# Optimization experiments

Measured on AMD Instinct MI355X. Metric: run time of the kernel, lower is better.

## Reference

```python
import jax, jax.numpy as jnp
import numpy as np

NUM_SAMPLES = 32  # S: Gibbs chains per datapoint


def setup_inputs() -> dict:
    key = jax.random.key(0)
    ks = jax.random.split(key, 6)
    N, F, M, C = 2048, 1024, 128, 100
    x = jax.random.normal(ks[0], (N, F), dtype=jnp.float32)
    y = jax.random.randint(ks[1], (N,), 0, C)
    alpha_0 = jax.random.normal(ks[2], (M,), dtype=jnp.float32)
    alpha = jax.random.normal(ks[3], (M, F), dtype=jnp.float32) * jnp.float32(2.0 / np.sqrt(F))
    beta_0 = jax.random.normal(ks[4], (C,), dtype=jnp.float32)
    beta = jax.random.normal(ks[5], (C, M), dtype=jnp.float32) * jnp.float32(2.0 / np.sqrt(M))
    return {"x": x, "y": y, "alpha_0": alpha_0, "alpha": alpha, "beta_0": beta_0, "beta": beta}


def _gibbs_and_loglik(x, y, alpha_0, alpha, beta_0, beta):
    S = NUM_SAMPLES
    N = x.shape[0]
    C, M = beta.shape
    y_onehot = jax.nn.one_hot(y, C, dtype=x.dtype)           # (N, C)

    # compute_linear_pi / compute_pi_pos (pi_pos is no_grad in original)
    linear_pi = alpha_0[None, :] + x @ alpha.T               # (N, M)
    pi_pos = jax.lax.stop_gradient(jax.nn.sigmoid(linear_pi))

    key = jax.random.key(42)
    k_init, k_gibbs = jax.random.split(key)

    # init_sample2: Z ~ 2*Bernoulli(pi_pos) - 1, sampled S times  (no_grad)
    Z0 = 2.0 * jax.random.bernoulli(k_init, pi_pos, (S, N, M)).astype(x.dtype) - 1.0

    beta_sg = jax.lax.stop_gradient(beta)
    beta0_sg = jax.lax.stop_gradient(beta_0)

    # class logits for current Z; maintained incrementally across Gibbs steps
    lin0 = beta0_sg[None, None, :] + jnp.einsum('snm,cm->snc', Z0, beta_sg)  # (S, N, C)

    order = jnp.asarray(np.random.RandomState(0).permutation(M))  # fixed Gibbs sweep order
    keys = jax.random.split(k_gibbs, M)

    def step(carry, inp):
        Z, lin = carry
        j, k = inp
        zj = jnp.take(Z, j, axis=2)           # (S, N) current value of coord j
        bj = jnp.take(beta_sg, j, axis=1)     # (C,)
        pij = jnp.take(pi_pos, j, axis=1)     # (N,)
        # logits if coord j were +1 / -1 (rank-1 update of lin)
        lin_pos = lin + (1.0 - zj)[..., None] * bj
        lin_neg = lin + (-1.0 - zj)[..., None] * bj
        g_pos = jnp.exp(jnp.einsum('nc,snc->sn', y_onehot, lin_pos)) / jnp.sum(jnp.exp(lin_pos), axis=2)
        g_neg = jnp.exp(jnp.einsum('nc,snc->sn', y_onehot, lin_neg)) / jnp.sum(jnp.exp(lin_neg), axis=2)
        num = g_pos * pij[None, :]
        p = num / (num + g_neg * (1.0 - pij)[None, :])
        znew = 2.0 * jax.random.bernoulli(k, p).astype(lin.dtype) - 1.0  # (S, N)
        lin = lin + (znew - zj)[..., None] * bj
        Z = jax.lax.dynamic_update_index_in_dim(Z, znew, j, axis=2)
        return (Z, lin), None

    (Z, _), _ = jax.lax.scan(step, (Z0, lin0), (order, keys))
    Z = jax.lax.stop_gradient(Z)

    # moments
    EI = jnp.mean((Z + 1.0) * 0.5, axis=0)                   # (N, M)
    EII = jnp.mean(Z, axis=0)                                # (N, M)
    linear_gamma = beta_0[None, None, :] + jnp.einsum('snm,cm->snc', Z, beta)
    EIII = jnp.mean(jax.nn.logsumexp(linear_gamma, axis=2), axis=0)  # (N,)

    TermI = jnp.sum(y_onehot * (beta_0[None, :] + EII @ beta.T))
    TermII = jnp.sum(EIII)
    TermIII = jnp.sum(EI * linear_pi)
    TermIV = jnp.sum(jax.nn.softplus(linear_pi))             # log(1 + exp(linear_pi)), stable
    return TermI - TermII + TermIII - TermIV


def reference(x, y, alpha_0, alpha, beta_0, beta):
    return _gibbs_and_loglik(x, y, alpha_0, alpha, beta_0, beta)
```

## Files before the change

### kernel.cpp

```cpp
#include <hip/hip_runtime.h>
#include <hip/hip_fp16.h>
#include <stdint.h>

#define Nn 2048
#define Ff 1024
#define Mm 128
#define Cc 100
#define Ss 32
#define NM (Nn * Mm)
#define ELS 132
#define SCP 128
#define TOFF 16400
#define ESC 0.015625f
#define ESCLOG 4.15888308336f

typedef short bf8 __attribute__((ext_vector_type(8)));
typedef float f32x4 __attribute__((ext_vector_type(4)));

__device__ __forceinline__ uint32_t hash32(uint32_t chain, uint32_t ctr) {
  uint32_t h = chain * 0x9E3779B9u ^ (ctr * 0x85EBCA6Bu);
  h ^= h >> 16; h *= 0x7FEB352Du;
  h ^= h >> 15; h *= 0x846CA68Bu;
  h ^= h >> 16;
  return h;
}
__device__ __forceinline__ float urand(uint32_t chain, uint32_t ctr) {
  return (float)(hash32(chain, ctr) >> 8) * (1.0f / 16777216.0f);
}
__device__ __forceinline__ uint32_t f2bf(float f) {
  uint32_t b = __builtin_bit_cast(uint32_t, f);
  return (b + 0x7FFFu + ((b >> 16) & 1u)) >> 16;
}
__device__ __forceinline__ float bf2f(uint16_t u) {
  uint32_t b = ((uint32_t)u) << 16;
  return __builtin_bit_cast(float, b);
}
__device__ __forceinline__ int cperm(int c) {
  return ((c >> 2) & 3) * 32 + (c >> 4) * 4 + (c & 3);
}

__global__ __launch_bounds__(256) void k_lingemm(const float* __restrict__ x,
                                                 const float* __restrict__ alpha,
                                                 uint16_t* __restrict__ lpib) {
  __shared__ uint4 sA[256];
  __shared__ uint4 sB[1024];
  const int t = threadIdx.x;
  const int mt = blockIdx.x >> 2;
  const int ks = blockIdx.x & 3;
  const int m0 = mt * 32;
  const int w = t >> 6;
  const int l = t & 63;

  f32x4 acc[2][2] = {{{0.f, 0.f, 0.f, 0.f}, {0.f, 0.f, 0.f, 0.f}},
                     {{0.f, 0.f, 0.f, 0.f}, {0.f, 0.f, 0.f, 0.f}}};

  for (int kk = 0; kk < 4; ++kk) {
    const int k0 = ks * 256 + kk * 64;
    __syncthreads();
    {
      int row = t >> 3, c = t & 7;
      const float* px = &x[(m0 + row) * Ff + k0 + c * 8];
      float4 f0 = *(const float4*)px;
      float4 f1 = *(const float4*)(px + 4);
      uint4 v;
      v.x = f2bf(f0.x) | (f2bf(f0.y) << 16);
      v.y = f2bf(f0.z) | (f2bf(f0.w) << 16);
      v.z = f2bf(f1.x) | (f2bf(f1.y) << 16);
      v.w = f2bf(f1.z) | (f2bf(f1.w) << 16);
      sA[row * 8 + (c ^ (row & 7))] = v;
      #pragma unroll
      for (int rr = 0; rr < 4; ++rr) {
        int idx = t + rr * 256;
        int rowb = idx >> 3, cb = idx & 7;
        const float* pa = &alpha[rowb * Ff + k0 + cb * 8];
        float4 g0 = *(const float4*)pa;
        float4 g1 = *(const float4*)(pa + 4);
        uint4 vb;
        vb.x = f2bf(g0.x) | (f2bf(g0.y) << 16);
        vb.y = f2bf(g0.z) | (f2bf(g0.w) << 16);
        vb.z = f2bf(g1.x) | (f2bf(g1.y) << 16);
        vb.w = f2bf(g1.z) | (f2bf(g1.w) << 16);
        sB[rowb * 8 + (cb ^ (rowb & 7))] = vb;
      }
    }
    __syncthreads();
    #pragma unroll
    for (int kc = 0; kc < 2; ++kc) {
      int chunk = kc * 4 + (l >> 4);
      bf8 av[2], bv[2];
      #pragma unroll
      for (int fm = 0; fm < 2; ++fm) {
        int row = fm * 16 + (l & 15);
        av[fm] = __builtin_bit_cast(bf8, sA[row * 8 + (chunk ^ (row & 7))]);
      }
      #pragma unroll
      for (int fn = 0; fn < 2; ++fn) {
        int rowb = w * 32 + fn * 16 + (l & 15);
        bv[fn] = __builtin_bit_cast(bf8, sB[rowb * 8 + (chunk ^ (rowb & 7))]);
      }
      #pragma unroll
      for (int fm = 0; fm < 2; ++fm)
        #pragma unroll
        for (int fn = 0; fn < 2; ++fn)
          acc[fm][fn] = __builtin_amdgcn_mfma_f32_16x16x32_bf16(av[fm], bv[fn], acc[fm][fn], 0, 0, 0);
    }
  }
  #pragma unroll
  for (int fm = 0; fm < 2; ++fm)
    #pragma unroll
    for (int fn = 0; fn < 2; ++fn)
      #pragma unroll
      for (int r = 0; r < 4; ++r) {
        int row = m0 + fm * 16 + (l >> 4) * 4 + r;
        int col = w * 32 + fn * 16 + (l & 15);
        lpib[ks * NM + row * Mm + col] = (uint16_t)f2bf(acc[fm][fn][r]);
      }
}

__global__ __launch_bounds__(512, 4) void k_gibbs(const float* __restrict__ beta0g,
                                                  const float* __restrict__ betag,
                                                  const int* __restrict__ yg,
                                                  const float* __restrict__ alpha0,
                                                  const uint16_t* __restrict__ lpib,
                                                  float* __restrict__ out) {
  __shared__ __attribute__((aligned(16))) char SM[74384];
  uint16_t* bsb = (uint16_t*)SM;
  float* b0p = (float*)(SM + 28672);
  __half* tab = (__half*)SM;
  float* elpi = (float*)(SM + 65600);
  float* lpil = (float*)(SM + 67712);
  uint32_t* zsl = (uint32_t*)(SM + 69760);
  float* lsel = (float*)(SM + 71808);
  float* red = (float*)(SM + 72320);
  int* yl = (int*)(SM + 74368);
  const int t = threadIdx.x;
  const int n0 = blockIdx.x * 4;
  const int lane = t & 63;

  for (int idx = t; idx < 112 * 32; idx += 512) {
    int row = idx >> 5, c4 = (idx & 31) * 4;
    float4 v = *(const float4*)&betag[row * Mm + c4];
    uint2 o;
    o.x = f2bf(v.x) | (f2bf(v.y) << 16);
    o.y = f2bf(v.z) | (f2bf(v.w) << 16);
    *(uint2*)&bsb[row * 128 + c4] = o;
  }
  if (t < 128) {
    b0p[cperm(t)] = (t < Cc) ? beta0g[t] : 0.0f;
  }
  {
    int nls = t >> 7, j = t & 127;
    int g = (n0 + nls) * Mm + j;
    float lv = bf2f(lpib[g]) + bf2f(lpib[NM + g]) + bf2f(lpib[2 * NM + g]) +
               bf2f(lpib[3 * NM + g]) + alpha0[j];
    lpil[nls * Mm + j] = lv;
    elpi[nls * ELS + j] = __expf(lv);
  }
  if (t < 4) yl[t] = yg[n0 + t];
  __syncthreads();

  const int li = lane & 15;
  const int h = lane >> 4;
  const int cl = (t >> 6) * 16 + li;
  const int nl = cl >> 5;
  const int s = cl & 31;
  const uint32_t chain = (uint32_t)((n0 + nl) * Ss + s);
  const int c0 = h * 32;
  const int yv = yl[nl];
  const int pyv = cperm(yv);

  uint32_t zw0, zw1, zw2, zw3;
  {
    uint32_t zz = 0;
    #pragma unroll 1
    for (int b5 = 0; b5 < 32; ++b5) {
      int mloc = (b5 + h * 8) & 31;
      int m = h * 32 + mloc;
      float u = urand(chain, (uint32_t)m);
      float el = elpi[nl * ELS + m];
      zz |= (u * (1.0f + el) < el) ? (1u << mloc) : 0u;
    }
    zw0 = (uint32_t)__shfl((int)zz, li + 0);
    zw1 = (uint32_t)__shfl((int)zz, li + 16);
    zw2 = (uint32_t)__shfl((int)zz, li + 32);
    zw3 = (uint32_t)__shfl((int)zz, li + 48);
  }

  f32x4 acc[7];
  #pragma unroll
  for (int T = 0; T < 7; ++T) acc[T] = (f32x4){0.f, 0.f, 0.f, 0.f};
  #pragma unroll
  for (int ks = 0; ks < 4; ++ks) {
    uint32_t zw = (ks == 0) ? zw0 : ((ks == 1) ? zw1 : ((ks == 2) ? zw2 : zw3));
    uint32_t bits8 = (zw >> (h * 8)) & 0xFFu;
    uint4 pk;
    {
      uint32_t p0 = ((bits8 >> 0) & 1u) ? 0x3F80u : 0xBF80u;
      uint32_t p1 = ((bits8 >> 1) & 1u) ? 0x3F80u : 0xBF80u;
      uint32_t p2 = ((bits8 >> 2) & 1u) ? 0x3F80u : 0xBF80u;
      uint32_t p3 = ((bits8 >> 3) & 1u) ? 0x3F80u : 0xBF80u;
      uint32_t p4 = ((bits8 >> 4) & 1u) ? 0x3F80u : 0xBF80u;
      uint32_t p5 = ((bits8 >> 5) & 1u) ? 0x3F80u : 0xBF80u;
      uint32_t p6 = ((bits8 >> 6) & 1u) ? 0x3F80u : 0xBF80u;
      uint32_t p7 = ((bits8 >> 7) & 1u) ? 0x3F80u : 0xBF80u;
      pk.x = p0 | (p1 << 16); pk.y = p2 | (p3 << 16);
      pk.z = p4 | (p5 << 16); pk.w = p6 | (p7 << 16);
    }
    bf8 B = __builtin_bit_cast(bf8, pk);
    #pragma unroll
    for (int T = 0; T < 7; ++T) {
      bf8 A = __builtin_bit_cast(bf8, *(const uint4*)&bsb[(T * 16 + li) * 128 + ks * 32 + h * 8]);
      acc[T] = __builtin_amdgcn_mfma_f32_16x16x32_bf16(A, B, acc[T], 0, 0, 0);
    }
  }

  const __half2 HZERO = __builtin_bit_cast(__half2, 0u);
  __half2 E2[16];
  #pragma unroll
  for (int k = 0; k < 14; ++k) {
    float2 b0v = *(const float2*)&b0p[c0 + 2 * k];
    float ea = __expf(acc[(2 * k) >> 2][(2 * k) & 3] + b0v.x) * ESC;
    float eb = __expf(acc[(2 * k + 1) >> 2][(2 * k + 1) & 3] + b0v.y) * ESC;
    E2[k] = __floats2half2_rn(ea, eb);
  }
  E2[14] = HZERO; E2[15] = HZERO;
  if (h != 0) { E2[12] = HZERO; E2[13] = HZERO; }

  float Sb;
  {
    const __half2 one2 = __floats2half2_rn(1.0f, 1.0f);
    __half2 a0 = HZERO, a1 = HZERO, a2 = HZERO, a3 = HZERO;
    #pragma unroll
    for (int k = 0; k < 4; ++k) {
      a0 = __hfma2(E2[4 * k + 0], one2, a0);
      a1 = __hfma2(E2[4 * k + 1], one2, a1);
      a2 = __hfma2(E2[4 * k + 2], one2, a2);
      a3 = __hfma2(E2[4 * k + 3], one2, a3);
    }
    __half2 sv = __hadd2(__hadd2(a0, a1), __hadd2(a2, a3));
    float d = __low2float(sv) + __high2float(sv);
    float d1 = d + __shfl_xor(d, 16);
    Sb = d1 + __shfl_xor(d1, 32);
  }

  __syncthreads();
  for (int idx = t; idx < 32 * Cc; idx += 512) {
    int j4 = idx / Cc;
    int c = idx - j4 * Cc;
    int p = cperm(c);
    float4 bv = *(const float4*)&betag[c * Mm + j4 * 4];
    int j = j4 * 4;
    tab[(j + 0) * SCP + p] = __float2half(__expf(2.0f * bv.x));
    tab[TOFF + (j + 0) * SCP + p] = __float2half(__expf(-2.0f * bv.x));
    tab[(j + 1) * SCP + p] = __float2half(__expf(2.0f * bv.y));
    tab[TOFF + (j + 1) * SCP + p] = __float2half(__expf(-2.0f * bv.y));
    tab[(j + 2) * SCP + p] = __float2half(__expf(2.0f * bv.z));
    tab[TOFF + (j + 2) * SCP + p] = __float2half(__expf(-2.0f * bv.z));
    tab[(j + 3) * SCP + p] = __float2half(__expf(2.0f * bv.w));
    tab[TOFF + (j + 3) * SCP + p] = __float2half(__expf(-2.0f * bv.w));
  }
  for (int idx = t; idx < Mm * 28; idx += 512) {
    int j = idx / 28;
    int c = Cc + (idx - j * 28);
    int p = cperm(c);
    tab[j * SCP + p] = __float2half(1.0f);
    tab[TOFF + j * SCP + p] = __float2half(1.0f);
  }
  __syncthreads();

  uint4 va[4], vb[4];
  auto pf = [&](uint4 (&dst)[4], uint32_t bit, int j) {
    const uint4* p4 = (const uint4*)(tab + (bit ? TOFF : 0) + j * SCP + c0);
    dst[0] = p4[0]; dst[1] = p4[1]; dst[2] = p4[2]; dst[3] = p4[3];
  };
  auto step = [&](uint4 (&v)[4], uint32_t zjp, float eyel, float u) -> uint32_t {
    __half2 a0 = HZERO, a1 = HZERO, a2 = HZERO, a3 = HZERO;
    #pragma unroll
    for (int k = 0; k < 4; ++k) {
      a0 = __hfma2(E2[4 * k + 0], __builtin_bit_cast(__half2, v[k].x), a0);
      a1 = __hfma2(E2[4 * k + 1], __builtin_bit_cast(__half2, v[k].y), a1);
      a2 = __hfma2(E2[4 * k + 2], __builtin_bit_cast(__half2, v[k].z), a2);
      a3 = __hfma2(E2[4 * k + 3], __builtin_bit_cast(__half2, v[k].w), a3);
    }
    __half2 sv = __hadd2(__hadd2(a0, a1), __hadd2(a2, a3));
    float d = __low2float(sv) + __high2float(sv);
    float d1 = d + __shfl_xor(d, 16);
    float D = d1 + __shfl_xor(d1, 32);
    float Spos = zjp ? Sb : D;
    float Sneg = zjp ? D : Sb;
    float odds = eyel * Sneg * __builtin_amdgcn_rcpf(Spos);
    uint32_t znp = (u * (1.0f + odds) < odds) ? 1u : 0u;
    if ((znp ^ zjp) != 0u) {
      #pragma unroll
      for (int k = 0; k < 4; ++k) {
        E2[4 * k + 0] = __hmul2(E2[4 * k + 0], __builtin_bit_cast(__half2, v[k].x));
        E2[4 * k + 1] = __hmul2(E2[4 * k + 1], __builtin_bit_cast(__half2, v[k].y));
        E2[4 * k + 2] = __hmul2(E2[4 * k + 2], __builtin_bit_cast(__half2, v[k].z));
        E2[4 * k + 3] = __hmul2(E2[4 * k + 3], __builtin_bit_cast(__half2, v[k].w));
      }
      Sb = D;
    }
    return znp;
  };

  pf(va, zw0 & 1u, 0);

  #pragma unroll 1
  for (int jb = 0; jb < Mm; jb += 4) {
    int w = jb >> 5;
    uint32_t zwv = (w == 0) ? zw0 : ((w == 1) ? zw1 : ((w == 2) ? zw2 : zw3));
    const int sh = jb & 31;
    uint32_t b0 = (zwv >> (sh + 0)) & 1u;
    uint32_t b1 = (zwv >> (sh + 1)) & 1u;
    uint32_t b2 = (zwv >> (sh + 2)) & 1u;
    uint32_t b3 = (zwv >> (sh + 3)) & 1u;
    uint32_t b4;
    if (sh == 28) {
      uint32_t nw = (w == 0) ? zw1 : ((w == 1) ? zw2 : ((w == 2) ? zw3 : 0u));
      b4 = nw & 1u;
    } else {
      b4 = (zwv >> (sh + 4)) & 1u;
    }
    float4 elv = *(const float4*)&elpi[nl * ELS + jb];
    float eyel0 = __half2float(tab[(jb + 0) * SCP + pyv]) * elv.x;
    float eyel1 = __half2float(tab[(jb + 1) * SCP + pyv]) * elv.y;
    float eyel2 = __half2float(tab[(jb + 2) * SCP + pyv]) * elv.z;
    float eyel3 = __half2float(tab[(jb + 3) * SCP + pyv]) * elv.w;
    uint32_t h1 = hash32(chain, 256u + (uint32_t)jb);
    uint32_t h2 = hash32(chain, 258u + (uint32_t)jb);
    float u0 = (float)(h1 & 0xFFFFu) * (1.0f / 65536.0f);
    float u1 = (float)(h1 >> 16) * (1.0f / 65536.0f);
    float u2 = (float)(h2 & 0xFFFFu) * (1.0f / 65536.0f);
    float u3 = (float)(h2 >> 16) * (1.0f / 65536.0f);

    pf(vb, b1, jb + 1);
    b0 = step(va, b0, eyel0, u0);
    pf(va, b2, jb + 2);
    b1 = step(vb, b1, eyel1, u1);
    pf(vb, b3, jb + 3);
    b2 = step(va, b2, eyel2, u2);
    pf(va, b4, (jb + 4) & 127);
    b3 = step(vb, b3, eyel3, u3);

    uint32_t nib = b0 | (b1 << 1) | (b2 << 2) | (b3 << 3);
    zwv = (zwv & ~(0xFu << sh)) | (nib << sh);
    if (w == 0) zw0 = zwv; else if (w == 1) zw1 = zwv;
    else if (w == 2) zw2 = zwv; else zw3 = zwv;
  }

  float Sf;
  {
    const __half2 one2 = __floats2half2_rn(1.0f, 1.0f);
    __half2 a0 = HZERO, a1 = HZERO, a2 = HZERO, a3 = HZERO;
    #pragma unroll
    for (int k = 0; k < 4; ++k) {
      a0 = __hfma2(E2[4 * k + 0], one2, a0);
      a1 = __hfma2(E2[4 * k + 1], one2, a1);
      a2 = __hfma2(E2[4 * k + 2], one2, a2);
      a3 = __hfma2(E2[4 * k + 3], one2, a3);
    }
    __half2 sv = __hadd2(__hadd2(a0, a1), __hadd2(a2, a3));
    float d = __low2float(sv) + __high2float(sv);
    float d1 = d + __shfl_xor(d, 16);
    Sf = d1 + __shfl_xor(d1, 32);
  }
  if (h == 0) {
    lsel[cl] = __logf(Sf) + ESCLOG;
    zsl[cl * 4 + 0] = zw0; zsl[cl * 4 + 1] = zw1;
    zsl[cl * 4 + 2] = zw2; zsl[cl * 4 + 3] = zw3;
  }
  __syncthreads();

  {
    int nl2 = t >> 7;
    int mp = t & 127;
    int wsel = mp >> 5, sh0 = mp & 31;
    int cnt = 0;
    #pragma unroll 1
    for (int s2 = 0; s2 < 32; ++s2)
      cnt += (int)((zsl[(nl2 * 32 + s2) * 4 + wsel] >> sh0) & 1u);
    float EI = (float)cnt * (1.0f / 32.0f);
    float EII = 2.0f * EI - 1.0f;
    float l = lpil[nl2 * Mm + mp];
    int yv2 = yl[nl2];
    float bb = betag[yv2 * Mm + mp];
    float sp = (l > 20.0f) ? l : __logf(1.0f + __expf(l));
    float term = EII * bb + EI * l - sp;
    if (t < 128) term -= lsel[t] * (1.0f / 32.0f);
    if (t < 4) term += beta0g[yl[t]];
    red[t] = term;
  }
  __syncthreads();
  for (int off = 256; off > 0; off >>= 1) {
    if (t < off) red[t] += red[t + off];
    __syncthreads();
  }
  if (t == 0) atomicAdd(out, red[0]);
}

extern "C" void kernel_launch(void* const* d_in, const int* in_sizes, int n_in,
                              void* d_out, int out_size, void* d_ws, size_t ws_size,
                              hipStream_t stream) {
  const float* x = (const float*)d_in[0];
  const int* y = (const int*)d_in[1];
  const float* alpha0 = (const float*)d_in[2];
  const float* alpha = (const float*)d_in[3];
  const float* beta0 = (const float*)d_in[4];
  const float* beta = (const float*)d_in[5];
  float* out = (float*)d_out;

  uint16_t* lpib = (uint16_t*)d_ws;

  hipMemsetAsync(d_out, 0, sizeof(float), stream);
  k_lingemm<<<256, 256, 0, stream>>>(x, alpha, lpib);
  k_gibbs<<<512, 512, 0, stream>>>(beta0, beta, y, alpha0, lpib, out);
}
```

Baseline: 104.0 us.

## Remap Gibbs chains to 4 adjacent lanes with DPP reductions and fdot2

Each Gibbs chain now lives on 4 adjacent lanes instead of 4 lanes strided by 16. That lets the per-step class-sum reduction use two DPP quad ops instead of two cross-lane shuffles. Half2 FMA accumulation is replaced with fdot2 into float accumulators, and the exp(±2β) table layout is swizzled per quarter-window to avoid LDS bank conflicts. Blocks grow to 1024 threads covering 8 datapoints, which needs more LDS per block and may reduce occupancy. The E2 values are redistributed with extra shuffles after the MFMA init.

Result: no change. 103.1 us (-0.8%).

```diff
diff --git a/kernel.cpp b/kernel.cpp
--- a/kernel.cpp
+++ b/kernel.cpp
@@ -10,12 +10,28 @@
 #define NM (Nn * Mm)
 #define ELS 132
 #define SCP 128
-#define TOFF 16400
+#define TOFF 16416
 #define ESC 0.015625f
 #define ESCLOG 4.15888308336f
 
+typedef _Float16 h2f __attribute__((ext_vector_type(2)));
 typedef short bf8 __attribute__((ext_vector_type(8)));
 typedef float f32x4 __attribute__((ext_vector_type(4)));
+
+__device__ __forceinline__ float qsum4(float x) {
+  int a = __builtin_amdgcn_update_dpp(0, __builtin_bit_cast(int, x), 0xB1, 0xF, 0xF, false);
+  float xf = x + __builtin_bit_cast(float, a);
+  int b = __builtin_amdgcn_update_dpp(0, __builtin_bit_cast(int, xf), 0x4E, 0xF, 0xF, false);
+  return xf + __builtin_bit_cast(float, b);
+}
+
+__device__ __forceinline__ float dot2f(h2f a, h2f b, float c) {
+#if __has_builtin(__builtin_amdgcn_fdot2)
+  return __builtin_amdgcn_fdot2(a, b, c, false);
+#else
+  return fmaf((float)a[0], (float)b[0], fmaf((float)a[1], (float)b[1], c));
+#endif
+}
 
 __device__ __forceinline__ uint32_t hash32(uint32_t chain, uint32_t ctr) {
   uint32_t h = chain * 0x9E3779B9u ^ (ctr * 0x85EBCA6Bu);
@@ -37,6 +53,10 @@
 }
 __device__ __forceinline__ int cperm(int c) {
   return ((c >> 2) & 3) * 32 + (c >> 4) * 4 + (c & 3);
+}
+__device__ __forceinline__ int swz(int p) {
+  int win = p >> 5, o = p & 31;
+  return win * 32 + (((o >> 3) + win) & 3) * 8 + (o & 7);
 }
 
 __global__ __launch_bounds__(256) void k_lingemm(const float* __restrict__ x,
@@ -117,37 +137,37 @@
       }
 }
 
-__global__ __launch_bounds__(512, 4) void k_gibbs(const float* __restrict__ beta0g,
-                                                  const float* __restrict__ betag,
-                                                  const int* __restrict__ yg,
-                                                  const float* __restrict__ alpha0,
-                                                  const uint16_t* __restrict__ lpib,
-                                                  float* __restrict__ out) {
-  __shared__ __attribute__((aligned(16))) char SM[74384];
+__global__ __launch_bounds__(1024, 4) void k_gibbs(const float* __restrict__ beta0g,
+                                                   const float* __restrict__ betag,
+                                                   const int* __restrict__ yg,
+                                                   const float* __restrict__ alpha0,
+                                                   const uint16_t* __restrict__ lpib,
+                                                   float* __restrict__ out) {
+  __shared__ __attribute__((aligned(16))) char SM[79584];
   uint16_t* bsb = (uint16_t*)SM;
-  float* b0p = (float*)(SM + 28672);
   __half* tab = (__half*)SM;
   float* elpi = (float*)(SM + 65600);
-  float* lpil = (float*)(SM + 67712);
-  uint32_t* zsl = (uint32_t*)(SM + 69760);
-  float* lsel = (float*)(SM + 71808);
-  float* red = (float*)(SM + 72320);
-  int* yl = (int*)(SM + 74368);
+  float* lpil = (float*)(SM + 69824);
+  uint32_t* zsl = (uint32_t*)(SM + 73920);
+  float* lsel = (float*)(SM + 78016);
+  int* yl = (int*)(SM + 79040);
+  float* b0p = (float*)(SM + 79072);
+  float* red = (float*)(SM + 65600);
+
   const int t = threadIdx.x;
-  const int n0 = blockIdx.x * 4;
-  const int lane = t & 63;
-
-  for (int idx = t; idx < 112 * 32; idx += 512) {
+  const int n0 = blockIdx.x * 8;
+  const int L = t & 63;
+
+  for (int idx = t; idx < 112 * 32; idx += 1024) {
     int row = idx >> 5, c4 = (idx & 31) * 4;
-    float4 v = *(const float4*)&betag[row * Mm + c4];
+    int rr = (row < Cc) ? row : 0;
+    float4 v = *(const float4*)&betag[rr * Mm + c4];
     uint2 o;
     o.x = f2bf(v.x) | (f2bf(v.y) << 16);
     o.y = f2bf(v.z) | (f2bf(v.w) << 16);
     *(uint2*)&bsb[row * 128 + c4] = o;
   }
-  if (t < 128) {
-    b0p[cperm(t)] = (t < Cc) ? beta0g[t] : 0.0f;
-  }
+  if (t < 128) b0p[cperm(t)] = (t < Cc) ? beta0g[t] : 0.0f;
   {
     int nls = t >> 7, j = t & 127;
     int g = (n0 + nls) * Mm + j;
@@ -156,34 +176,26 @@
     lpil[nls * Mm + j] = lv;
     elpi[nls * ELS + j] = __expf(lv);
   }
-  if (t < 4) yl[t] = yg[n0 + t];
+  if (t < 8) yl[t] = yg[n0 + t];
   __syncthreads();
 
-  const int li = lane & 15;
-  const int h = lane >> 4;
-  const int cl = (t >> 6) * 16 + li;
+  const int cl = t >> 2;
+  const int hq = t & 3;
   const int nl = cl >> 5;
   const int s = cl & 31;
   const uint32_t chain = (uint32_t)((n0 + nl) * Ss + s);
-  const int c0 = h * 32;
   const int yv = yl[nl];
-  const int pyv = cperm(yv);
-
-  uint32_t zw0, zw1, zw2, zw3;
-  {
-    uint32_t zz = 0;
+
+  uint32_t zz = 0;
+  {
     #pragma unroll 1
     for (int b5 = 0; b5 < 32; ++b5) {
-      int mloc = (b5 + h * 8) & 31;
-      int m = h * 32 + mloc;
+      int mloc = (b5 + hq * 8) & 31;
+      int m = hq * 32 + mloc;
       float u = urand(chain, (uint32_t)m);
       float el = elpi[nl * ELS + m];
       zz |= (u * (1.0f + el) < el) ? (1u << mloc) : 0u;
     }
-    zw0 = (uint32_t)__shfl((int)zz, li + 0);
-    zw1 = (uint32_t)__shfl((int)zz, li + 16);
-    zw2 = (uint32_t)__shfl((int)zz, li + 32);
-    zw3 = (uint32_t)__shfl((int)zz, li + 48);
   }
 
   f32x4 acc[7];
@@ -191,8 +203,8 @@
   for (int T = 0; T < 7; ++T) acc[T] = (f32x4){0.f, 0.f, 0.f, 0.f};
   #pragma unroll
   for (int ks = 0; ks < 4; ++ks) {
-    uint32_t zw = (ks == 0) ? zw0 : ((ks == 1) ? zw1 : ((ks == 2) ? zw2 : zw3));
-    uint32_t bits8 = (zw >> (h * 8)) & 0xFFu;
+    uint32_t zw = (uint32_t)__shfl((int)zz, ((L & 15) << 2) | ks, 64);
+    uint32_t bits8 = (zw >> ((L >> 4) * 8)) & 0xFFu;
     uint4 pk;
     {
       uint32_t p0 = ((bits8 >> 0) & 1u) ? 0x3F80u : 0xBF80u;
@@ -209,83 +221,98 @@
     bf8 B = __builtin_bit_cast(bf8, pk);
     #pragma unroll
     for (int T = 0; T < 7; ++T) {
-      bf8 A = __builtin_bit_cast(bf8, *(const uint4*)&bsb[(T * 16 + li) * 128 + ks * 32 + h * 8]);
+      bf8 A = __builtin_bit_cast(bf8, *(const uint4*)&bsb[(T * 16 + (L & 15)) * 128 + ks * 32 + (L >> 4) * 8]);
       acc[T] = __builtin_amdgcn_mfma_f32_16x16x32_bf16(A, B, acc[T], 0, 0, 0);
     }
   }
 
   const __half2 HZERO = __builtin_bit_cast(__half2, 0u);
   __half2 E2[16];
-  #pragma unroll
-  for (int k = 0; k < 14; ++k) {
-    float2 b0v = *(const float2*)&b0p[c0 + 2 * k];
-    float ea = __expf(acc[(2 * k) >> 2][(2 * k) & 3] + b0v.x) * ESC;
-    float eb = __expf(acc[(2 * k + 1) >> 2][(2 * k + 1) & 3] + b0v.y) * ESC;
-    E2[k] = __floats2half2_rn(ea, eb);
-  }
-  E2[14] = HZERO; E2[15] = HZERO;
-  if (h != 0) { E2[12] = HZERO; E2[13] = HZERO; }
-
+  {
+    int c0m = (L >> 4) * 32;
+    #pragma unroll
+    for (int k = 0; k < 14; ++k) {
+      float2 b0v = *(const float2*)&b0p[c0m + 2 * k];
+      float ea = __expf(acc[(2 * k) >> 2][(2 * k) & 3] + b0v.x) * ESC;
+      float eb = __expf(acc[(2 * k + 1) >> 2][(2 * k + 1) & 3] + b0v.y) * ESC;
+      E2[k] = __floats2half2_rn(ea, eb);
+    }
+    E2[14] = HZERO; E2[15] = HZERO;
+    if ((L >> 4) != 0) { E2[12] = HZERO; E2[13] = HZERO; }
+  }
+
+  {
+    int src = (L >> 2) | ((L & 3) << 4);
+    #pragma unroll
+    for (int k = 0; k < 14; ++k)
+      E2[k] = __builtin_bit_cast(__half2, (uint32_t)__shfl((int)__builtin_bit_cast(uint32_t, E2[k]), src, 64));
+  }
+  uint32_t zw0 = (uint32_t)__shfl((int)zz, (L & ~3) | 0, 64);
+  uint32_t zw1 = (uint32_t)__shfl((int)zz, (L & ~3) | 1, 64);
+  uint32_t zw2 = (uint32_t)__shfl((int)zz, (L & ~3) | 2, 64);
+  uint32_t zw3 = (uint32_t)__shfl((int)zz, (L & ~3) | 3, 64);
+
+  const h2f one2 = {(_Float16)1.0f, (_Float16)1.0f};
   float Sb;
   {
-    const __half2 one2 = __floats2half2_rn(1.0f, 1.0f);
-    __half2 a0 = HZERO, a1 = HZERO, a2 = HZERO, a3 = HZERO;
-    #pragma unroll
-    for (int k = 0; k < 4; ++k) {
-      a0 = __hfma2(E2[4 * k + 0], one2, a0);
-      a1 = __hfma2(E2[4 * k + 1], one2, a1);
-      a2 = __hfma2(E2[4 * k + 2], one2, a2);
-      a3 = __hfma2(E2[4 * k + 3], one2, a3);
-    }
-    __half2 sv = __hadd2(__hadd2(a0, a1), __hadd2(a2, a3));
-    float d = __low2float(sv) + __high2float(sv);
-    float d1 = d + __shfl_xor(d, 16);
-    Sb = d1 + __shfl_xor(d1, 32);
+    float d0 = 0.f, d1 = 0.f;
+    #pragma unroll
+    for (int k = 0; k < 16; ++k) {
+      if (k & 1) d1 = dot2f(__builtin_bit_cast(h2f, E2[k]), one2, d1);
+      else d0 = dot2f(__builtin_bit_cast(h2f, E2[k]), one2, d0);
+    }
+    Sb = qsum4(d0 + d1);
   }
 
   __syncthreads();
-  for (int idx = t; idx < 32 * Cc; idx += 512) {
+  for (int idx = t; idx < 32 * Cc; idx += 1024) {
     int j4 = idx / Cc;
     int c = idx - j4 * Cc;
-    int p = cperm(c);
+    int ps = swz(cperm(c));
     float4 bv = *(const float4*)&betag[c * Mm + j4 * 4];
     int j = j4 * 4;
-    tab[(j + 0) * SCP + p] = __float2half(__expf(2.0f * bv.x));
-    tab[TOFF + (j + 0) * SCP + p] = __float2half(__expf(-2.0f * bv.x));
-    tab[(j + 1) * SCP + p] = __float2half(__expf(2.0f * bv.y));
-    tab[TOFF + (j + 1) * SCP + p] = __float2half(__expf(-2.0f * bv.y));
-    tab[(j + 2) * SCP + p] = __float2half(__expf(2.0f * bv.z));
-    tab[TOFF + (j + 2) * SCP + p] = __float2half(__expf(-2.0f * bv.z));
-    tab[(j + 3) * SCP + p] = __float2half(__expf(2.0f * bv.w));
-    tab[TOFF + (j + 3) * SCP + p] = __float2half(__expf(-2.0f * bv.w));
-  }
-  for (int idx = t; idx < Mm * 28; idx += 512) {
+    tab[(j + 0) * SCP + ps] = __float2half(__expf(2.0f * bv.x));
+    tab[TOFF + (j + 0) * SCP + ps] = __float2half(__expf(-2.0f * bv.x));
+    tab[(j + 1) * SCP + ps] = __float2half(__expf(2.0f * bv.y));
+    tab[TOFF + (j + 1) * SCP + ps] = __float2half(__expf(-2.0f * bv.y));
+    tab[(j + 2) * SCP + ps] = __float2half(__expf(2.0f * bv.z));
+    tab[TOFF + (j + 2) * SCP + ps] = __float2half(__expf(-2.0f * bv.z));
+    tab[(j + 3) * SCP + ps] = __float2half(__expf(2.0f * bv.w));
+    tab[TOFF + (j + 3) * SCP + ps] = __float2half(__expf(-2.0f * bv.w));
+  }
+  for (int idx = t; idx < Mm * 28; idx += 1024) {
     int j = idx / 28;
     int c = Cc + (idx - j * 28);
-    int p = cperm(c);
-    tab[j * SCP + p] = __float2half(1.0f);
-    tab[TOFF + j * SCP + p] = __float2half(1.0f);
+    int ps = swz(cperm(c));
+    tab[j * SCP + ps] = __float2half(1.0f);
+    tab[TOFF + j * SCP + ps] = __float2half(1.0f);
   }
   __syncthreads();
+
+  const int pyv_s = swz(cperm(yv));
+  const int rot0 = ((0 + hq) & 3) * 8;
+  const int rot1 = ((1 + hq) & 3) * 8;
+  const int rot2 = ((2 + hq) & 3) * 8;
+  const int rot3 = ((3 + hq) & 3) * 8;
 
   uint4 va[4], vb[4];
   auto pf = [&](uint4 (&dst)[4], uint32_t bit, int j) {
-    const uint4* p4 = (const uint4*)(tab + (bit ? TOFF : 0) + j * SCP + c0);
-    dst[0] = p4[0]; dst[1] = p4[1]; dst[2] = p4[2]; dst[3] = p4[3];
+    const __half* p = tab + (bit ? TOFF : 0) + j * SCP + hq * 32;
+    dst[0] = *(const uint4*)(p + rot0);
+    dst[1] = *(const uint4*)(p + rot1);
+    dst[2] = *(const uint4*)(p + rot2);
+    dst[3] = *(const uint4*)(p + rot3);
   };
   auto step = [&](uint4 (&v)[4], uint32_t zjp, float eyel, float u) -> uint32_t {
-    __half2 a0 = HZERO, a1 = HZERO, a2 = HZERO, a3 = HZERO;
+    float d0 = 0.f, d1 = 0.f, d2 = 0.f, d3 = 0.f;
     #pragma unroll
     for (int k = 0; k < 4; ++k) {
-      a0 = __hfma2(E2[4 * k + 0], __builtin_bit_cast(__half2, v[k].x), a0);
-      a1 = __hfma2(E2[4 * k + 1], __builtin_bit_cast(__half2, v[k].y), a1);
-      a2 = __hfma2(E2[4 * k + 2], __builtin_bit_cast(__half2, v[k].z), a2);
-      a3 = __hfma2(E2[4 * k + 3], __builtin_bit_cast(__half2, v[k].w), a3);
-    }
-    __half2 sv = __hadd2(__hadd2(a0, a1), __hadd2(a2, a3));
-    float d = __low2float(sv) + __high2float(sv);
-    float d1 = d + __shfl_xor(d, 16);
-    float D = d1 + __shfl_xor(d1, 32);
+      d0 = dot2f(__builtin_bit_cast(h2f, E2[4 * k + 0]), __builtin_bit_cast(h2f, v[k].x), d0);
+      d1 = dot2f(__builtin_bit_cast(h2f, E2[4 * k + 1]), __builtin_bit_cast(h2f, v[k].y), d1);
+      d2 = dot2f(__builtin_bit_cast(h2f, E2[4 * k + 2]), __builtin_bit_cast(h2f, v[k].z), d2);
+      d3 = dot2f(__builtin_bit_cast(h2f, E2[4 * k + 3]), __builtin_bit_cast(h2f, v[k].w), d3);
+    }
+    float D = qsum4((d0 + d1) + (d2 + d3));
     float Spos = zjp ? Sb : D;
     float Sneg = zjp ? D : Sb;
     float odds = eyel * Sneg * __builtin_amdgcn_rcpf(Spos);
@@ -322,10 +349,10 @@
       b4 = (zwv >> (sh + 4)) & 1u;
     }
     float4 elv = *(const float4*)&elpi[nl * ELS + jb];
-    float eyel0 = __half2float(tab[(jb + 0) * SCP + pyv]) * elv.x;
-    float eyel1 = __half2float(tab[(jb + 1) * SCP + pyv]) * elv.y;
-    float eyel2 = __half2float(tab[(jb + 2) * SCP + pyv]) * elv.z;
-    float eyel3 = __half2float(tab[(jb + 3) * SCP + pyv]) * elv.w;
+    float eyel0 = __half2float(tab[(jb + 0) * SCP + pyv_s]) * elv.x;
+    float eyel1 = __half2float(tab[(jb + 1) * SCP + pyv_s]) * elv.y;
+    float eyel2 = __half2float(tab[(jb + 2) * SCP + pyv_s]) * elv.z;
+    float eyel3 = __half2float(tab[(jb + 3) * SCP + pyv_s]) * elv.w;
     uint32_t h1 = hash32(chain, 256u + (uint32_t)jb);
     uint32_t h2 = hash32(chain, 258u + (uint32_t)jb);
     float u0 = (float)(h1 & 0xFFFFu) * (1.0f / 65536.0f);
@@ -350,21 +377,15 @@
 
   float Sf;
   {
-    const __half2 one2 = __floats2half2_rn(1.0f, 1.0f);
-    __half2 a0 = HZERO, a1 = HZERO, a2 = HZERO, a3 = HZERO;
-    #pragma unroll
-    for (int k = 0; k < 4; ++k) {
-      a0 = __hfma2(E2[4 * k + 0], one2, a0);
-      a1 = __hfma2(E2[4 * k + 1], one2, a1);
-      a2 = __hfma2(E2[4 * k + 2], one2, a2);
-      a3 = __hfma2(E2[4 * k + 3], one2, a3);
-    }
-    __half2 sv = __hadd2(__hadd2(a0, a1), __hadd2(a2, a3));
-    float d = __low2float(sv) + __high2float(sv);
-    float d1 = d + __shfl_xor(d, 16);
-    Sf = d1 + __shfl_xor(d1, 32);
-  }
-  if (h == 0) {
+    float d0 = 0.f, d1 = 0.f;
+    #pragma unroll
+    for (int k = 0; k < 16; ++k) {
+      if (k & 1) d1 = dot2f(__builtin_bit_cast(h2f, E2[k]), one2, d1);
+      else d0 = dot2f(__builtin_bit_cast(h2f, E2[k]), one2, d0);
+    }
+    Sf = qsum4(d0 + d1);
+  }
+  if (hq == 0) {
     lsel[cl] = __logf(Sf) + ESCLOG;
     zsl[cl * 4 + 0] = zw0; zsl[cl * 4 + 1] = zw1;
     zsl[cl * 4 + 2] = zw2; zsl[cl * 4 + 3] = zw3;
@@ -386,12 +407,12 @@
     float bb = betag[yv2 * Mm + mp];
     float sp = (l > 20.0f) ? l : __logf(1.0f + __expf(l));
     float term = EII * bb + EI * l - sp;
-    if (t < 128) term -= lsel[t] * (1.0f / 32.0f);
-    if (t < 4) term += beta0g[yl[t]];
+    if (t < 256) term -= lsel[t] * (1.0f / 32.0f);
+    if (t < 8) term += beta0g[yl[t]];
     red[t] = term;
   }
   __syncthreads();
-  for (int off = 256; off > 0; off >>= 1) {
+  for (int off = 512; off > 0; off >>= 1) {
     if (t < off) red[t] += red[t + off];
     __syncthreads();
   }
@@ -413,5 +434,5 @@
 
   hipMemsetAsync(d_out, 0, sizeof(float), stream);
   k_lingemm<<<256, 256, 0, stream>>>(x, alpha, lpib);
-  k_gibbs<<<512, 512, 0, stream>>>(beta0, beta, y, alpha0, lpib, out);
-}
+  k_gibbs<<<256, 1024, 0, stream>>>(beta0, beta, y, alpha0, lpib, out);
+}
```
